# Performance work log

Hardware: AMD Instinct MI355X
Metric: run time of the kernel (lower is better)

Reference implementation:

```python
import jax, jax.numpy as jnp
import numpy as np

INDIM = 1024
NHEADS = 16
DK = INDIM // NHEADS  # 64
DV = INDIM // NHEADS  # 64
B, S = 4, 2048


def setup_inputs() -> dict:
    key = jax.random.key(0)
    ks = jax.random.split(key, 5)
    x = jax.random.normal(ks[0], (B, S, INDIM), dtype=jnp.float32)
    std_qk = np.sqrt(2.0 / (INDIM + DK)).astype(np.float32)
    std_v = np.sqrt(2.0 / (INDIM + DV)).astype(np.float32)
    Wq = jax.random.normal(ks[1], (NHEADS * DK, INDIM), dtype=jnp.float32) * std_qk
    Wk = jax.random.normal(ks[2], (NHEADS * DK, INDIM), dtype=jnp.float32) * std_qk
    Wv = jax.random.normal(ks[3], (NHEADS * DV, INDIM), dtype=jnp.float32) * std_v
    # xavier normal for output proj
    std_o = np.sqrt(2.0 / (NHEADS * DV + INDIM)).astype(np.float32)
    Wo = jax.random.normal(ks[4], (INDIM, NHEADS * DV), dtype=jnp.float32) * std_o
    bq = jnp.zeros((NHEADS * DK,), jnp.float32)
    bk = jnp.zeros((NHEADS * DK,), jnp.float32)
    bv = jnp.zeros((NHEADS * DV,), jnp.float32)
    bo = jnp.zeros((INDIM,), jnp.float32)
    return {"x": x, "Wq": Wq, "bq": bq, "Wk": Wk, "bk": bk, "Wv": Wv, "bv": bv, "Wo": Wo, "bo": bo}


def reference(x, Wq, bq, Wk, bk, Wv, bv, Wo, bo):
    b, s, _ = x.shape
    q = (x @ Wq.T + bq).reshape(b, s, NHEADS, DK)
    k = (x @ Wk.T + bk).reshape(b, s, NHEADS, DK)
    v = (x @ Wv.T + bv).reshape(b, s, NHEADS, DV)
    # scores: [b, h, s, z]
    w = jnp.einsum('bshd,bzhd->bhsz', q, k)
    # original divides by sqrt(d_v) (v.size(-1)) when scale=True
    w = w / jnp.sqrt(jnp.float32(DV))
    w = jax.nn.softmax(w, axis=-1)
    vw = jnp.einsum('bhsz,bzhd->bshd', w, v)  # [b, s, h, dv]
    vw = vw.reshape(b, s, NHEADS * DV)
    out = vw @ Wo.T + bo
    return out
```

## Files before the change

kernel.cpp:

```cpp
#include <hip/hip_runtime.h>
#include <hip/hip_bf16.h>
#include <cstdint>
#include <cstddef>

#define NHEADS 16
#define HDIM   64
#define SEQ    2048
#define BATCH  4
#define IND    1024
#define MTOT   (BATCH*SEQ)

typedef __attribute__((ext_vector_type(8))) short bf16x8;
typedef __attribute__((ext_vector_type(8))) _Float16 f16x8;
typedef __attribute__((ext_vector_type(4))) float f32x4;
typedef __attribute__((ext_vector_type(16))) float f32x16;
typedef __attribute__((ext_vector_type(2))) int i32x2;
typedef __attribute__((ext_vector_type(4))) unsigned u32x4;

#if __has_builtin(__builtin_amdgcn_exp2f)
#define EXP2(x) __builtin_amdgcn_exp2f(x)
#else
#define EXP2(x) exp2f(x)
#endif

__device__ __forceinline__ unsigned short f2b(float f) {
  unsigned u = __builtin_bit_cast(unsigned, f);
  u += 0x7FFFu + ((u >> 16) & 1u);
  return (unsigned short)(u >> 16);
}
__device__ __forceinline__ unsigned cvt2(float lo, float hi) {
  float2 t; t.x = lo; t.y = hi;
  __hip_bfloat162 h = __float22bfloat162_rn(t);
  const unsigned short ulo = __bfloat16_as_ushort(h.x);
  const unsigned short uhi = __bfloat16_as_ushort(h.y);
  return (unsigned)ulo | ((unsigned)uhi << 16);
}
__device__ __forceinline__ unsigned pkrtz(float lo, float hi) {
  return __builtin_bit_cast(unsigned, __builtin_amdgcn_cvt_pkrtz(lo, hi));
}
__device__ __forceinline__ float m3(float a, float b, float c) {
  return fmaxf(fmaxf(a, b), c);
}

__device__ __forceinline__ void gload_lds16(const void* g, void* l) {
  __builtin_amdgcn_global_load_lds(
      (const __attribute__((address_space(1))) void*)g,
      (__attribute__((address_space(3))) void*)l, 16, 0, 0);
}

__global__ void cvt_kernel(const float* __restrict__ src,
                           unsigned short* __restrict__ dst, int n4) {
  int i = blockIdx.x * blockDim.x + threadIdx.x;
  const int stride = gridDim.x * blockDim.x;
  for (; i < n4; i += stride) {
    const float4 v = reinterpret_cast<const float4*>(src)[i];
    ushort4 o;
    o.x = f2b(v.x); o.y = f2b(v.y); o.z = f2b(v.z); o.w = f2b(v.w);
    reinterpret_cast<ushort4*>(dst)[i] = o;
  }
}

__global__ void cvtw_kernel(const float* __restrict__ w0, const float* __restrict__ w1,
                            const float* __restrict__ w2, const float* __restrict__ w3,
                            unsigned short* __restrict__ o0, unsigned short* __restrict__ o1,
                            unsigned short* __restrict__ o2, unsigned short* __restrict__ o3,
                            int n4) {
  const int z = blockIdx.y;
  const float* src = (z == 0) ? w0 : (z == 1) ? w1 : (z == 2) ? w2 : w3;
  unsigned short* dst = (z == 0) ? o0 : (z == 1) ? o1 : (z == 2) ? o2 : o3;
  int i = blockIdx.x * blockDim.x + threadIdx.x;
  const int stride = gridDim.x * blockDim.x;
  for (; i < n4; i += stride) {
    const float4 v = reinterpret_cast<const float4*>(src)[i];
    ushort4 o;
    o.x = f2b(v.x); o.y = f2b(v.y); o.z = f2b(v.z); o.w = f2b(v.w);
    reinterpret_cast<ushort4*>(dst)[i] = o;
  }
}

template<int EPI>
__device__ __forceinline__ void gemm_core(
    const unsigned short* __restrict__ A,
    const unsigned short* __restrict__ Bw,
    const float* __restrict__ bias,
    void* __restrict__ Cout, float scale)
{
  __shared__ alignas(16) unsigned short As[2][4096];
  __shared__ alignas(16) unsigned short Bs[2][4096];
  const int tid = threadIdx.x;
  const int wv = tid >> 6, lane = tid & 63, g = lane >> 4, li = lane & 15;
  const int wr = (wv >> 1) * 64, wc = (wv & 1) * 64;
  const int m0 = blockIdx.x * 128, n0 = blockIdx.y * 128;

  auto stage = [&](int buf, int kt) {
    const int k0 = kt * 32;
#pragma unroll
    for (int rnd = 0; rnd < 2; ++rnd) {
      const int f = (tid + rnd * 256) * 8;
      const int row = f >> 5, col = f & 31;
      gload_lds16(&A[(size_t)(m0 + row) * IND + k0 + col], &As[buf][f]);
      gload_lds16(&Bw[(size_t)(n0 + row) * IND + k0 + col], &Bs[buf][f]);
    }
  };

  f32x4 acc[4][4] = {};
  stage(0, 0);
  for (int kt = 0; kt < 32; ++kt) {
    __syncthreads();
    if (kt + 1 < 32) stage((kt + 1) & 1, kt + 1);
    const int buf = kt & 1;
    bf16x8 af[4], bfr[4];
#pragma unroll
    for (int i = 0; i < 4; ++i)
      af[i] = *(const bf16x8*)&As[buf][(wr + i * 16 + li) * 32 + g * 8];
#pragma unroll
    for (int i = 0; i < 4; ++i)
      bfr[i] = *(const bf16x8*)&Bs[buf][(wc + i * 16 + li) * 32 + g * 8];
#pragma unroll
    for (int mi = 0; mi < 4; ++mi)
#pragma unroll
      for (int ni = 0; ni < 4; ++ni) {
        if (EPI == 2)
          acc[mi][ni] = __builtin_amdgcn_mfma_f32_16x16x32_bf16(
              bfr[ni], af[mi], acc[mi][ni], 0, 0, 0);
        else
          acc[mi][ni] = __builtin_amdgcn_mfma_f32_16x16x32_bf16(
              af[mi], bfr[ni], acc[mi][ni], 0, 0, 0);
      }
  }

  if (EPI == 2) {
#pragma unroll
    for (int ni = 0; ni < 4; ++ni) {
#pragma unroll
      for (int r = 0; r < 4; ++r) {
        const int n = n0 + wc + ni * 16 + g * 4 + r;
        const float bz = bias[n];
        const int h = n >> 6, d = n & 63;
#pragma unroll
        for (int mi = 0; mi < 4; ++mi) {
          const int tok = m0 + wr + mi * 16 + li;
          const int b = tok >> 11, s = tok & 2047;
          const float v = acc[mi][ni][r] + bz;
          ((_Float16*)Cout)[(((size_t)(b * NHEADS + h)) * HDIM + d) * SEQ + s] =
              (_Float16)v;
        }
      }
    }
  } else {
#pragma unroll
    for (int ni = 0; ni < 4; ++ni) {
      const int col = n0 + wc + ni * 16 + li;
      const float bz = bias[col];
#pragma unroll
      for (int mi = 0; mi < 4; ++mi) {
#pragma unroll
        for (int r = 0; r < 4; ++r) {
          const int row = m0 + wr + mi * 16 + g * 4 + r;
          float v = acc[mi][ni][r] + bz;
          if (EPI == 0) {
            v *= scale;
            const int h = col >> 6, d = col & 63;
            const int b = row >> 11, s = row & 2047;
            ((unsigned short*)Cout)[(((size_t)(b * NHEADS + h)) * SEQ + s) * HDIM + d] = f2b(v);
          } else {
            ((float*)Cout)[(size_t)row * IND + col] = v;
          }
        }
      }
    }
  }
}

__global__ __launch_bounds__(256, 2)
void gemm_qkv_kernel(const unsigned short* __restrict__ xb,
                     const unsigned short* __restrict__ Wq,
                     const unsigned short* __restrict__ Wk,
                     const unsigned short* __restrict__ Wv,
                     const float* __restrict__ bq,
                     const float* __restrict__ bk,
                     const float* __restrict__ bv,
                     unsigned short* __restrict__ Qo,
                     unsigned short* __restrict__ Ko,
                     unsigned short* __restrict__ Vto)
{
  const int z = blockIdx.z;
  if (z == 2) {
    gemm_core<2>(xb, Wv, bv, Vto, 1.0f);
  } else {
    const unsigned short* Bw = (z == 0) ? Wq : Wk;
    const float* bias = (z == 0) ? bq : bk;
    unsigned short* out = (z == 0) ? Qo : Ko;
    const float scale = (z == 0) ? 0.18033688011111772f : 1.0f;
    gemm_core<0>(xb, Bw, bias, out, scale);
  }
}

__global__ __launch_bounds__(256, 2)
void gemm_o_kernel(const unsigned short* __restrict__ Ab,
                   const unsigned short* __restrict__ Wo,
                   const float* __restrict__ bo,
                   float* __restrict__ out)
{
  gemm_core<1>(Ab, Wo, bo, out, 1.0f);
}

__global__ __launch_bounds__(256, 4)
void attn_kernel(const unsigned short* __restrict__ Q,
                 const unsigned short* __restrict__ K,
                 const unsigned short* __restrict__ Vt,
                 unsigned short* __restrict__ U0,
                 unsigned short* __restrict__ U1,
                 float* __restrict__ Ml,
                 float* __restrict__ Ll)
{
  __shared__ alignas(16) unsigned short Kb[2][32 * 64];
  __shared__ alignas(16) unsigned short Vb[2][64 * 32];

  const int tid = threadIdx.x;
  const int wv = tid >> 6, lane = tid & 63;
  const int r31 = lane & 31, hi = lane >> 5;

  const unsigned flat = blockIdx.x;
  const unsigned wg = (flat & 7) * 256 + (flat >> 3);
  const int qblk = wg & 15;
  const int bh = (wg >> 4) & 63;
  const int split = wg >> 10;
  const int koff = split * 1024;

  const size_t hbase = (size_t)bh * (SEQ * HDIM);
  const unsigned short* Qh = Q + hbase;
  const unsigned short* Kh = K + hbase;
  const unsigned short* Vh = Vt + hbase;
  const int q0 = qblk * 128 + wv * 32;

  bf16x8 qf[4];
#pragma unroll
  for (int kc = 0; kc < 4; ++kc)
    qf[kc] = *(const bf16x8*)&Qh[(size_t)(q0 + r31) * HDIM + kc * 16 + hi * 8];

  f32x16 accO[2] = {};
  float m_run = -INFINITY, l_run = 0.0f;

  auto stage = [&](int buf, int kv) {
    const int k0 = koff + kv * 32;
    {
      const int row = tid >> 3, pch = tid & 7;
      const int ch = pch ^ (row & 7);
      gload_lds16(&Kh[(size_t)(k0 + row) * HDIM + ch * 8], &Kb[buf][tid * 8]);
    }
    {
      const int row = tid >> 2, pch = tid & 3;
      const int ch = pch ^ ((row >> 1) & 3);
      gload_lds16(&Vh[(size_t)row * SEQ + k0 + ch * 8], &Vb[buf][tid * 8]);
    }
  };

  stage(0, 0);

  for (int kv = 0; kv < 32; ++kv) {
    __syncthreads();
    if (kv + 1 < 32) stage((kv + 1) & 1, kv + 1);
    const int buf = kv & 1;

    f32x16 s0 = {};
#pragma unroll
    for (int kc = 0; kc < 4; ++kc) {
      const int pch = (kc * 2 + hi) ^ (r31 & 7);
      const bf16x8 kf = *(const bf16x8*)&Kb[buf][r31 * 64 + pch * 8];
      s0 = __builtin_amdgcn_mfma_f32_32x32x16_bf16(kf, qf[kc], s0, 0, 0, 0);
    }

    float t0 = m3(s0[0], s0[1], s0[2]),  t1 = m3(s0[3], s0[4], s0[5]);
    float t2 = m3(s0[6], s0[7], s0[8]),  t3 = m3(s0[9], s0[10], s0[11]);
    float t4 = m3(s0[12], s0[13], s0[14]);
    float pmax = m3(m3(t0, t1, s0[15]), fmaxf(t2, t3), t4);
    pmax = fmaxf(pmax, __shfl_xor(pmax, 32));

    if (!__all(pmax - m_run <= 8.0f)) {
      const float mn = fmaxf(m_run, pmax);
      const float al = EXP2(m_run - mn);
      l_run *= al;
#pragma unroll
      for (int f = 0; f < 2; ++f)
#pragma unroll
        for (int r = 0; r < 16; ++r) accO[f][r] *= al;
      m_run = mn;
    }

    unsigned pk[8];
    float rs = 0.0f;
#pragma unroll
    for (int i = 0; i < 8; ++i) {
      const float ea = EXP2(s0[2 * i] - m_run);
      const float eb = EXP2(s0[2 * i + 1] - m_run);
      rs += ea + eb;
      pk[i] = pkrtz(ea, eb);
    }
    rs += __shfl_xor(rs, 32);
    l_run += rs;

    f16x8 pf[2];
#pragma unroll
    for (int kc2 = 0; kc2 < 2; ++kc2) {
      const int bs = kc2 * 4;
      const i32x2 rA = __builtin_amdgcn_permlane32_swap(
          (int)pk[bs + 0], (int)pk[bs + 2], false, false);
      const i32x2 rB = __builtin_amdgcn_permlane32_swap(
          (int)pk[bs + 1], (int)pk[bs + 3], false, false);
      u32x4 u;
      u[0] = (unsigned)rA[0];
      u[1] = (unsigned)rB[0];
      u[2] = (unsigned)rA[1];
      u[3] = (unsigned)rB[1];
      pf[kc2] = __builtin_bit_cast(f16x8, u);
    }

#pragma unroll
    for (int kc2 = 0; kc2 < 2; ++kc2) {
      const int vpch = (kc2 * 2 + hi) ^ ((r31 >> 1) & 3);
      const int vbase = r31 * 32 + vpch * 8;
      const f16x8 vf0 = *(const f16x8*)&Vb[buf][vbase];
      accO[0] = __builtin_amdgcn_mfma_f32_32x32x16_f16(vf0, pf[kc2], accO[0], 0, 0, 0);
      const f16x8 vf1 = *(const f16x8*)&Vb[buf][vbase + 1024];
      accO[1] = __builtin_amdgcn_mfma_f32_32x32x16_f16(vf1, pf[kc2], accO[1], 0, 0, 0);
    }
  }

  const int b = bh >> 4, h = bh & 15;
  const int qrow = q0 + r31;
  unsigned short* Up = (split == 0) ? U0 : U1;
  unsigned short* obase = &Up[((size_t)(b * SEQ + qrow)) * IND + h * HDIM];
#pragma unroll
  for (int f = 0; f < 2; ++f) {
#pragma unroll
    for (int half = 0; half < 4; ++half) {
      uint2 w;
      w.x = pkrtz(accO[f][half * 4 + 0], accO[f][half * 4 + 1]);
      w.y = pkrtz(accO[f][half * 4 + 2], accO[f][half * 4 + 3]);
      *(uint2*)&obase[32 * f + 8 * half + 4 * hi] = w;
    }
  }
  if (hi == 0) {
    Ml[((size_t)(split * 64 + bh)) * SEQ + qrow] = m_run;
    Ll[((size_t)(split * 64 + bh)) * SEQ + qrow] = l_run;
  }
}

__global__ __launch_bounds__(256, 4)
void combine_kernel(const unsigned short* U0h,
                    const unsigned short* __restrict__ U1h,
                    const float* __restrict__ Ml, const float* __restrict__ Ll,
                    unsigned short* O)
{
  const int bh = blockIdx.x;
  const int q0 = blockIdx.y * 128;
  const int tid = threadIdx.x;
  const int qq = q0 + (tid >> 1);
  const int dh = (tid & 1) * 32;
  const int b = bh >> 4, h = bh & 15;

  const float m0v = Ml[(size_t)bh * SEQ + qq];
  const float m1v = Ml[(size_t)(64 + bh) * SEQ + qq];
  const float l0 = Ll[(size_t)bh * SEQ + qq];
  const float l1 = Ll[(size_t)(64 + bh) * SEQ + qq];
  const float mm = fmaxf(m0v, m1v);
  const float a0 = EXP2(m0v - mm), a1 = EXP2(m1v - mm);
  const float inv = 1.0f / (l0 * a0 + l1 * a1);
  const float c0 = a0 * inv, c1 = a1 * inv;

  const size_t base = ((size_t)(b * SEQ + qq)) * IND + h * HDIM + dh;
#pragma unroll
  for (int it = 0; it < 4; ++it) {
    const f16x8 u0 = *(const f16x8*)&U0h[base + it * 8];
    const f16x8 u1 = *(const f16x8*)&U1h[base + it * 8];
    float o[8];
#pragma unroll
    for (int j = 0; j < 8; ++j)
      o[j] = (float)u0[j] * c0 + (float)u1[j] * c1;
    uint4 w;
    w.x = cvt2(o[0], o[1]); w.y = cvt2(o[2], o[3]);
    w.z = cvt2(o[4], o[5]); w.w = cvt2(o[6], o[7]);
    *(uint4*)&O[base + it * 8] = w;
  }
}

extern "C" void kernel_launch(void* const* d_in, const int* in_sizes, int n_in,
                              void* d_out, int out_size, void* d_ws, size_t ws_size,
                              hipStream_t stream) {
  const float* x  = (const float*)d_in[0];
  const float* Wq = (const float*)d_in[1];
  const float* bq = (const float*)d_in[2];
  const float* Wk = (const float*)d_in[3];
  const float* bk = (const float*)d_in[4];
  const float* Wv = (const float*)d_in[5];
  const float* bv = (const float*)d_in[6];
  const float* Wo = (const float*)d_in[7];
  const float* bo = (const float*)d_in[8];

  char* ws = (char*)d_ws;
  constexpr size_t SZ_XB = (size_t)MTOT * IND * 2;
  constexpr size_t SZ_W  = (size_t)IND * IND * 2;
  unsigned short* xb   = (unsigned short*)(ws);
  unsigned short* Wqb  = (unsigned short*)(ws + SZ_XB);
  unsigned short* Wkb  = (unsigned short*)(ws + SZ_XB + SZ_W);
  unsigned short* Wvb  = (unsigned short*)(ws + SZ_XB + 2 * SZ_W);
  unsigned short* Wob  = (unsigned short*)(ws + SZ_XB + 3 * SZ_W);
  unsigned short* Qb   = (unsigned short*)(ws + SZ_XB + 4 * SZ_W);
  unsigned short* Kbuf = (unsigned short*)(ws + 2 * SZ_XB + 4 * SZ_W);
  unsigned short* Vtb  = (unsigned short*)(ws + 3 * SZ_XB + 4 * SZ_W);
  unsigned short* AOb  = (unsigned short*)(ws + 4 * SZ_XB + 4 * SZ_W);

  unsigned short* U1   = xb;
  float*          Mlp  = (float*)Wqb;
  float*          Llp  = (float*)Wkb;

  cvt_kernel<<<2048, 256, 0, stream>>>(x, xb, (MTOT * IND) / 4);
  cvtw_kernel<<<dim3(512, 4), 256, 0, stream>>>(Wq, Wk, Wv, Wo,
                                                Wqb, Wkb, Wvb, Wob, (IND * IND) / 4);

  gemm_qkv_kernel<<<dim3(MTOT / 128, IND / 128, 3), 256, 0, stream>>>(
      xb, Wqb, Wkb, Wvb, bq, bk, bv, Qb, Kbuf, Vtb);

  attn_kernel<<<dim3(2048), 256, 0, stream>>>(Qb, Kbuf, Vtb, AOb, U1, Mlp, Llp);

  combine_kernel<<<dim3(BATCH * NHEADS, SEQ / 128), 256, 0, stream>>>(
      AOb, U1, Mlp, Llp, AOb);

  gemm_o_kernel<<<dim3(MTOT / 128, IND / 128), 256, 0, stream>>>(
      AOb, Wob, bo, (float*)d_out);
}
```

Baseline: 227.0 us.

## Double KV tile to 64, read V from global, compute row sums via MFMA

The attention inner loop now handles 64 keys per iteration instead of 32, which halves the number of barriers and loop iterations. V is no longer staged through LDS; each wave loads its V fragments directly from global memory. The softmax denominator is now produced by an extra MFMA against a ones vector instead of scalar adds plus a cross-lane shuffle. The trade-off is that V loads are no longer shared across the block through LDS, so their global latency may be exposed to the MFMA chain, and register pressure goes up from the larger tile and the extra accumulator.

```diff
diff --git a/kernel.cpp b/kernel.cpp
--- a/kernel.cpp
+++ b/kernel.cpp
@@ -214,8 +214,7 @@
                  float* __restrict__ Ml,
                  float* __restrict__ Ll)
 {
-  __shared__ alignas(16) unsigned short Kb[2][32 * 64];
-  __shared__ alignas(16) unsigned short Vb[2][64 * 32];
+  __shared__ alignas(16) unsigned short Kb[2][64 * 64];
 
   const int tid = threadIdx.x;
   const int wv = tid >> 6, lane = tid & 63;
@@ -231,7 +230,7 @@
   const size_t hbase = (size_t)bh * (SEQ * HDIM);
   const unsigned short* Qh = Q + hbase;
   const unsigned short* Kh = K + hbase;
-  const unsigned short* Vh = Vt + hbase;
+  const _Float16* Vh = (const _Float16*)(Vt + hbase);
   const int q0 = qblk * 128 + wv * 32;
 
   bf16x8 qf[4];
@@ -239,70 +238,86 @@
   for (int kc = 0; kc < 4; ++kc)
     qf[kc] = *(const bf16x8*)&Qh[(size_t)(q0 + r31) * HDIM + kc * 16 + hi * 8];
 
+  f16x8 onesA;
+  {
+    const _Float16 ov = (r31 == 0) ? (_Float16)1.0f : (_Float16)0.0f;
+#pragma unroll
+    for (int j = 0; j < 8; ++j) onesA[j] = ov;
+  }
+
   f32x16 accO[2] = {};
-  float m_run = -INFINITY, l_run = 0.0f;
+  f32x16 accL = {};
+  float m_run = -INFINITY;
 
   auto stage = [&](int buf, int kv) {
-    const int k0 = koff + kv * 32;
-    {
-      const int row = tid >> 3, pch = tid & 7;
+    const int k0 = koff + kv * 64;
+#pragma unroll
+    for (int rnd = 0; rnd < 2; ++rnd) {
+      const int c = tid + rnd * 256;
+      const int row = c >> 3, pch = c & 7;
       const int ch = pch ^ (row & 7);
-      gload_lds16(&Kh[(size_t)(k0 + row) * HDIM + ch * 8], &Kb[buf][tid * 8]);
-    }
-    {
-      const int row = tid >> 2, pch = tid & 3;
-      const int ch = pch ^ ((row >> 1) & 3);
-      gload_lds16(&Vh[(size_t)row * SEQ + k0 + ch * 8], &Vb[buf][tid * 8]);
+      gload_lds16(&Kh[(size_t)(k0 + row) * HDIM + ch * 8], &Kb[buf][c * 8]);
     }
   };
 
   stage(0, 0);
 
-  for (int kv = 0; kv < 32; ++kv) {
+  for (int kv = 0; kv < 16; ++kv) {
     __syncthreads();
-    if (kv + 1 < 32) stage((kv + 1) & 1, kv + 1);
+    if (kv + 1 < 16) stage((kv + 1) & 1, kv + 1);
     const int buf = kv & 1;
-
-    f32x16 s0 = {};
+    const int k0 = koff + kv * 64;
+
+    f32x16 s0 = {}, s1 = {};
 #pragma unroll
     for (int kc = 0; kc < 4; ++kc) {
       const int pch = (kc * 2 + hi) ^ (r31 & 7);
-      const bf16x8 kf = *(const bf16x8*)&Kb[buf][r31 * 64 + pch * 8];
-      s0 = __builtin_amdgcn_mfma_f32_32x32x16_bf16(kf, qf[kc], s0, 0, 0, 0);
-    }
-
-    float t0 = m3(s0[0], s0[1], s0[2]),  t1 = m3(s0[3], s0[4], s0[5]);
-    float t2 = m3(s0[6], s0[7], s0[8]),  t3 = m3(s0[9], s0[10], s0[11]);
+      const int base = r31 * 64 + pch * 8;
+      const bf16x8 kf0 = *(const bf16x8*)&Kb[buf][base];
+      s0 = __builtin_amdgcn_mfma_f32_32x32x16_bf16(kf0, qf[kc], s0, 0, 0, 0);
+      const bf16x8 kf1 = *(const bf16x8*)&Kb[buf][base + 2048];
+      s1 = __builtin_amdgcn_mfma_f32_32x32x16_bf16(kf1, qf[kc], s1, 0, 0, 0);
+    }
+
+    float t0 = m3(s0[0], s0[1], s0[2]),   t1 = m3(s0[3], s0[4], s0[5]);
+    float t2 = m3(s0[6], s0[7], s0[8]),   t3 = m3(s0[9], s0[10], s0[11]);
     float t4 = m3(s0[12], s0[13], s0[14]);
-    float pmax = m3(m3(t0, t1, s0[15]), fmaxf(t2, t3), t4);
+    float u0 = m3(t0, t1, s0[15]),        u1 = fmaxf(t2, fmaxf(t3, t4));
+    float t5 = m3(s1[0], s1[1], s1[2]),   t6 = m3(s1[3], s1[4], s1[5]);
+    float t7 = m3(s1[6], s1[7], s1[8]),   t8 = m3(s1[9], s1[10], s1[11]);
+    float t9 = m3(s1[12], s1[13], s1[14]);
+    float u2 = m3(t5, t6, s1[15]),        u3 = fmaxf(t7, fmaxf(t8, t9));
+    float pmax = m3(fmaxf(u0, u1), u2, u3);
     pmax = fmaxf(pmax, __shfl_xor(pmax, 32));
 
     if (!__all(pmax - m_run <= 8.0f)) {
       const float mn = fmaxf(m_run, pmax);
       const float al = EXP2(m_run - mn);
-      l_run *= al;
 #pragma unroll
       for (int f = 0; f < 2; ++f)
 #pragma unroll
         for (int r = 0; r < 16; ++r) accO[f][r] *= al;
+      accL[0] *= al;
       m_run = mn;
     }
 
-    unsigned pk[8];
-    float rs = 0.0f;
+    unsigned pk[16];
 #pragma unroll
     for (int i = 0; i < 8; ++i) {
       const float ea = EXP2(s0[2 * i] - m_run);
       const float eb = EXP2(s0[2 * i + 1] - m_run);
-      rs += ea + eb;
       pk[i] = pkrtz(ea, eb);
     }
-    rs += __shfl_xor(rs, 32);
-    l_run += rs;
-
-    f16x8 pf[2];
-#pragma unroll
-    for (int kc2 = 0; kc2 < 2; ++kc2) {
+#pragma unroll
+    for (int i = 0; i < 8; ++i) {
+      const float ea = EXP2(s1[2 * i] - m_run);
+      const float eb = EXP2(s1[2 * i + 1] - m_run);
+      pk[8 + i] = pkrtz(ea, eb);
+    }
+
+    f16x8 pf[4];
+#pragma unroll
+    for (int kc2 = 0; kc2 < 4; ++kc2) {
       const int bs = kc2 * 4;
       const i32x2 rA = __builtin_amdgcn_permlane32_swap(
           (int)pk[bs + 0], (int)pk[bs + 2], false, false);
@@ -317,15 +332,18 @@
     }
 
 #pragma unroll
-    for (int kc2 = 0; kc2 < 2; ++kc2) {
-      const int vpch = (kc2 * 2 + hi) ^ ((r31 >> 1) & 3);
-      const int vbase = r31 * 32 + vpch * 8;
-      const f16x8 vf0 = *(const f16x8*)&Vb[buf][vbase];
+    for (int kc2 = 0; kc2 < 4; ++kc2) {
+      const size_t vcol = (size_t)(k0 + kc2 * 16 + hi * 8);
+      const f16x8 vf0 = *(const f16x8*)&Vh[(size_t)r31 * SEQ + vcol];
       accO[0] = __builtin_amdgcn_mfma_f32_32x32x16_f16(vf0, pf[kc2], accO[0], 0, 0, 0);
-      const f16x8 vf1 = *(const f16x8*)&Vb[buf][vbase + 1024];
+      const f16x8 vf1 = *(const f16x8*)&Vh[(size_t)(32 + r31) * SEQ + vcol];
       accO[1] = __builtin_amdgcn_mfma_f32_32x32x16_f16(vf1, pf[kc2], accO[1], 0, 0, 0);
-    }
-  }
+      accL = __builtin_amdgcn_mfma_f32_32x32x16_f16(onesA, pf[kc2], accL, 0, 0, 0);
+    }
+  }
+
+  float lv = accL[0];
+  lv += __shfl_xor(lv, 32);
 
   const int b = bh >> 4, h = bh & 15;
   const int qrow = q0 + r31;
@@ -343,7 +361,7 @@
   }
   if (hi == 0) {
     Ml[((size_t)(split * 64 + bh)) * SEQ + qrow] = m_run;
-    Ll[((size_t)(split * 64 + bh)) * SEQ + qrow] = l_run;
+    Ll[((size_t)(split * 64 + bh)) * SEQ + qrow] = lv;
   }
 }
 
```

Result: slower. 271.0 us (+19.4%).
